# Kernel optimization log

Hardware: AMD Instinct MI355X
Metric: run time of the kernel (lower is better)

Reference implementation:

```python
import jax, jax.numpy as jnp
import numpy as np

B, CIN, COUT, K, SDIM, H, W = 16, 512, 512, 3, 512, 64, 64


def setup_inputs() -> dict:
    key = jax.random.key(0)
    k1, k2, k3, k4 = jax.random.split(key, 4)
    return {
        "x": jax.random.normal(k1, (B, CIN, H, W), dtype=jnp.float32),
        "style": jax.random.normal(k2, (B, SDIM), dtype=jnp.float32),
        "weight": jax.random.normal(k3, (COUT, CIN, K, K), dtype=jnp.float32),
        "style_w": jax.random.normal(k4, (CIN, SDIM), dtype=jnp.float32),
        "style_b": jnp.ones((CIN,), dtype=jnp.float32),  # bias.data.fill_(1.0)
    }


def reference(x, style, weight, style_w, style_b):
    batch, in_ch, h, w_size = x.shape
    out_ch, _, ks, _ = weight.shape
    pad = ks // 2
    # EqualizedLinear: runtime weight scaling by 1/sqrt(fan_in)
    lin_scale = 1.0 / np.sqrt(style_w.shape[1])
    s = style @ (style_w * lin_scale).T + style_b  # [B, Cin]
    # modulate
    conv_scale = 1.0 / np.sqrt(in_ch * ks * ks)
    wmod = (weight[None] * conv_scale) * s[:, None, :, None, None]  # [B,Cout,Cin,k,k]
    # demodulate
    dcoef = jax.lax.rsqrt(jnp.sum(jnp.square(wmod), axis=(2, 3, 4)) + 1e-8)  # [B,Cout]
    wmod = wmod * dcoef[:, :, None, None, None]
    # grouped conv with groups = batch
    x_r = x.reshape(1, batch * in_ch, h, w_size)
    w_r = wmod.reshape(batch * out_ch, in_ch, ks, ks)
    out = jax.lax.conv_general_dilated(
        x_r, w_r,
        window_strides=(1, 1),
        padding=[(pad, pad), (pad, pad)],
        dimension_numbers=("NCHW", "OIHW", "NCHW"),
        feature_group_count=batch,
    )
    return out.reshape(batch, out_ch, h, w_size)
```

## Files before the change

### kernel.cpp

```cpp
#include <hip/hip_runtime.h>
#include <math.h>

#define B 16
#define CIN 512
#define COUT 512
#define SDIM 512
#define H 64
#define W 64

typedef short s16x8 __attribute__((ext_vector_type(8)));
typedef float f32x4 __attribute__((ext_vector_type(4)));
typedef float f32x16 __attribute__((ext_vector_type(16)));

__device__ __constant__ float LIN_SCALE  = 0.04419417382415922f;
__device__ __constant__ float CONV_SCALE = 0.014731391274719742f;

__device__ __forceinline__ ushort f2bf(float f) {
  unsigned u = __float_as_uint(f);
  return (ushort)((u + 0x7FFFu + ((u >> 16) & 1u)) >> 16);
}

#define GLOAD16(g, l)                                           \
  __builtin_amdgcn_global_load_lds(                             \
      (const __attribute__((address_space(1))) unsigned*)(g),   \
      (__attribute__((address_space(3))) unsigned*)(l), 16, 0, 0)

__global__ __launch_bounds__(256) void prep1_kernel(
    const float* __restrict__ w, const float* __restrict__ style,
    const float* __restrict__ style_w, const float* __restrict__ style_b,
    ushort* __restrict__ wt, float* __restrict__ wsq, float* __restrict__ s,
    float* __restrict__ s2) {
  const int tid = threadIdx.x;
  if (blockIdx.x < 512) {
    const int u = blockIdx.x * 256 + tid;
    const int e = u & 7;
    const int chunk = (u >> 3) & 31;
    const int co = u >> 8;
    const float2* wp = (const float2*)(
        w + ((size_t)co * 512 + chunk * 16 + e * 2) * 9);
    float wv[18];
#pragma unroll
    for (int i = 0; i < 9; ++i) {
      float2 v = wp[i];
      wv[2 * i] = v.x;
      wv[2 * i + 1] = v.y;
    }
    {
      float q0 = 0.f, q1 = 0.f;
#pragma unroll
      for (int k = 0; k < 9; ++k) {
        q0 += wv[k] * wv[k];
        q1 += wv[9 + k] * wv[9 + k];
      }
      *(float2*)(wsq + (size_t)co * 512 + chunk * 16 + e * 2) =
          make_float2(q0, q1);
    }
    const int cb = co >> 6, co64 = co & 63;
    ushort* dst = wt + (size_t)chunk * 73728 + (size_t)cb * 9216 +
                  (size_t)(e >> 2) * 512 + (size_t)co64 * 8 + (e & 3) * 2;
#pragma unroll
    for (int j = 0; j < 9; ++j) {
      unsigned pk = (unsigned)f2bf(wv[j]) | ((unsigned)f2bf(wv[9 + j]) << 16);
      *(unsigned*)(dst + (size_t)j * 1024) = pk;
    }
  } else {
    const int bb = blockIdx.x - 512;
    __shared__ float st[SDIM];
    st[tid] = style[bb * SDIM + tid];
    st[tid + 256] = style[bb * SDIM + tid + 256];
    __syncthreads();
#pragma unroll
    for (int half = 0; half < 2; ++half) {
      const int ci = tid + half * 256;
      const float4* wr =
          reinterpret_cast<const float4*>(style_w + (size_t)ci * SDIM);
      float acc = 0.f;
#pragma unroll 4
      for (int k = 0; k < SDIM / 4; ++k) {
        float4 wv = wr[k];
        acc += st[4 * k + 0] * wv.x + st[4 * k + 1] * wv.y +
               st[4 * k + 2] * wv.z + st[4 * k + 3] * wv.w;
      }
      float v = acc * LIN_SCALE + style_b[ci];
      s[bb * CIN + ci] = v;
      s2[bb * CIN + ci] = v * v;
    }
  }
}

__global__ __launch_bounds__(256) void prep2_kernel(
    const float* __restrict__ x, const float* __restrict__ smod,
    const float* __restrict__ s2, const float* __restrict__ wsq,
    ushort* __restrict__ xp, float* __restrict__ outscale) {
  const int tid = threadIdx.x;
  if (blockIdx.x < 16384) {
    const int blk = blockIdx.x;
    const int gr = blk & 63, cp = (blk >> 6) & 15, b = blk >> 10;
    __shared__ float xt[32][65];
    __shared__ float sm[32];
    if (tid < 32) sm[tid] = smod[b * 512 + cp * 32 + tid];
    {
      const int ci = tid >> 3, cq = tid & 7;
      const float4* rp = (const float4*)(
          x + (((size_t)b * 512 + cp * 32 + ci) * 64 + gr) * 64 + cq * 8);
      float4 a = rp[0], c2 = rp[1];
      float* row = &xt[ci][cq * 8];
      row[0] = a.x; row[1] = a.y; row[2] = a.z; row[3] = a.w;
      row[4] = c2.x; row[5] = c2.y; row[6] = c2.z; row[7] = c2.w;
    }
    __syncthreads();
    const int c = tid & 63, o = tid >> 6;
    s16x8 p;
#pragma unroll
    for (int i = 0; i < 8; ++i)
      p[i] = (short)f2bf(xt[o * 8 + i][c] * sm[o * 8 + i]);
    const int chunk = cp * 2 + (o >> 1), oct = o & 1;
    *(s16x8*)(xp + (size_t)b * 2097152 + (size_t)chunk * 65536 +
              oct * 32768 + gr * 512 + c * 8) = p;
  } else {
    const int b = blockIdx.x - 16384;
    __shared__ float sh[CIN];
    sh[tid] = s2[b * CIN + tid];
    sh[tid + 256] = s2[b * CIN + tid + 256];
    __syncthreads();
#pragma unroll
    for (int half = 0; half < 2; ++half) {
      const int co = tid + half * 256;
      const float4* wr =
          reinterpret_cast<const float4*>(wsq + (size_t)co * CIN);
      float acc = 0.f;
#pragma unroll 4
      for (int k = 0; k < CIN / 4; ++k) {
        float4 wv = wr[k];
        acc += sh[4 * k + 0] * wv.x + sh[4 * k + 1] * wv.y +
               sh[4 * k + 2] * wv.z + sh[4 * k + 3] * wv.w;
      }
      float d = rsqrtf(acc * CONV_SCALE * CONV_SCALE + 1e-8f);
      outscale[b * COUT + co] = d * CONV_SCALE;
    }
  }
}

#define CBUF_WS 18432
#define CBUF_XS 21120
#define XS_BASE 36864
#define DLDS9 79104

__global__ __launch_bounds__(256, 2) void conv_mfma9_kernel(
    const ushort* __restrict__ wt, const ushort* __restrict__ xp,
    const float* __restrict__ outscale, float* __restrict__ out) {
  extern __shared__ char smem[];

  const int tid = threadIdx.x;
  const int hb = blockIdx.x;
  const int cb = blockIdx.y;
  const int b  = blockIdx.z;
  const int h0 = hb * 8, co0 = cb * 64;
  const int lane = tid & 63, wid = tid >> 6;
  const int l31 = lane & 31, hi = lane >> 5;

  {
    s16x8* p = (s16x8*)(smem + XS_BASE);
    for (int e = tid; e < 2640; e += 256) p[e] = (s16x8)0;
  }

  f32x16 acc[2][2][2];
#pragma unroll
  for (int rr = 0; rr < 2; ++rr)
#pragma unroll
    for (int mt = 0; mt < 2; ++mt)
#pragma unroll
      for (int nt = 0; nt < 2; ++nt) acc[rr][mt][nt] = (f32x16)0.f;

  int aoff[2];
#pragma unroll
  for (int mt = 0; mt < 2; ++mt)
    aoff[mt] = hi * 1024 + (mt * 32 + l31) * 16;
  int boff[3][2];
#pragma unroll
  for (int kw = 0; kw < 3; ++kw)
#pragma unroll
    for (int nt = 0; nt < 2; ++nt)
      boff[kw][nt] = hi * 10560 + (nt * 32 + l31 + kw) * 16;

  const char* wsrc0 = (const char*)wt + (size_t)cb * 18432;
  const char* xsrc0 = (const char*)xp + (size_t)b * 4194304;

  auto stage = [&](int chunk, int buf) {
    const char* wsrc = wsrc0 + (size_t)chunk * 147456;
    const char* xsrc = xsrc0 + (size_t)chunk * 131072;
    char* wd = smem + buf * CBUF_WS;
    char* xd = smem + XS_BASE + buf * CBUF_XS;
#pragma unroll
    for (int p = 0; p < 4; ++p)
      GLOAD16(wsrc + p * 4096 + tid * 16, wd + p * 4096 + tid * 16);
    if (tid < 128)
      GLOAD16(wsrc + 16384 + tid * 16, wd + 16384 + tid * 16);
#pragma unroll
    for (int p = 0; p < 5; ++p) {
      int e = p * 4 + wid;
      int oct = (e >= 10) ? 1 : 0;
      int r = e - oct * 10;
      int gr = h0 - 1 + r;
      if ((unsigned)gr < 64u)
        GLOAD16(xsrc + oct * 65536 + gr * 1024 + lane * 16,
                xd + oct * 10560 + r * 1056 + 16 + lane * 16);
    }
  };

  auto compute = [&](int buf) {
    const char* wb2 = smem + buf * CBUF_WS;
    const char* xb2 = smem + XS_BASE + buf * CBUF_XS + 2 * wid * 1056;
#pragma unroll
    for (int kw = 0; kw < 3; ++kw) {
      s16x8 bf[4][2];
#pragma unroll
      for (int q = 0; q < 4; ++q)
#pragma unroll
        for (int nt = 0; nt < 2; ++nt)
          bf[q][nt] = *(const s16x8*)(xb2 + q * 1056 + boff[kw][nt]);
#pragma unroll
      for (int kh = 0; kh < 3; ++kh) {
        const char* wj = wb2 + (kh * 3 + kw) * 2048;
        s16x8 af0 = *(const s16x8*)(wj + aoff[0]);
        s16x8 af1 = *(const s16x8*)(wj + aoff[1]);
#pragma unroll
        for (int rr = 0; rr < 2; ++rr)
#pragma unroll
          for (int nt = 0; nt < 2; ++nt) {
            acc[rr][0][nt] = __builtin_amdgcn_mfma_f32_32x32x16_bf16(
                af0, bf[rr + kh][nt], acc[rr][0][nt], 0, 0, 0);
            acc[rr][1][nt] = __builtin_amdgcn_mfma_f32_32x32x16_bf16(
                af1, bf[rr + kh][nt], acc[rr][1][nt], 0, 0, 0);
          }
      }
    }
  };

  __syncthreads();
  stage(0, 0);

  for (int c = 0; c < 32; ++c) {
    const int buf = c & 1;
    __syncthreads();
    if (c + 1 < 32) stage(c + 1, buf ^ 1);
    compute(buf);
  }

#pragma unroll
  for (int mt = 0; mt < 2; ++mt) {
#pragma unroll
    for (int reg = 0; reg < 16; ++reg) {
      const int row = (reg & 3) + 8 * (reg >> 2) + 4 * hi;
      const int co = co0 + mt * 32 + row;
      const float osc = outscale[b * COUT + co];
      float* obase = out + ((size_t)b * COUT + co) * H * W;
#pragma unroll
      for (int rr = 0; rr < 2; ++rr) {
        const int h = h0 + 2 * wid + rr;
#pragma unroll
        for (int nt = 0; nt < 2; ++nt)
          obase[h * W + nt * 32 + l31] = acc[rr][mt][nt][reg] * osc;
      }
    }
  }
}

__global__ __launch_bounds__(256, 2) void conv_mfma_kernel(
    const float* __restrict__ x, const float* __restrict__ weight,
    const float* __restrict__ s, const float* __restrict__ outscale,
    float* __restrict__ out) {
  __shared__ ushort xs[6][66][32];
  __shared__ ushort ws[9][64][32];

  const int tid = threadIdx.x;
  const int hb = blockIdx.x;
  const int cb = blockIdx.y;
  const int b  = blockIdx.z;
  const int h0 = hb * 4;
  const int co0 = cb * 64;
  const int lane = tid & 63;
  const int wid = tid >> 6;
  const int l15 = lane & 15;
  const int l4  = lane >> 4;

  f32x4 acc[4][4];
#pragma unroll
  for (int mt = 0; mt < 4; ++mt)
#pragma unroll
    for (int nt = 0; nt < 4; ++nt) acc[mt][nt] = (f32x4)0.f;

  const int wq = tid & 3;
  const int wco = tid >> 2;

  for (int c0 = 0; c0 < CIN; c0 += 32) {
    {
      const float4* wp = reinterpret_cast<const float4*>(
          weight + ((size_t)(co0 + wco) * CIN + c0 + wq * 8) * 9);
      float wv[72];
#pragma unroll
      for (int t = 0; t < 18; ++t) {
        float4 v = wp[t];
        wv[4 * t + 0] = v.x; wv[4 * t + 1] = v.y;
        wv[4 * t + 2] = v.z; wv[4 * t + 3] = v.w;
      }
      float sv[8];
#pragma unroll
      for (int i = 0; i < 8; ++i) sv[i] = s[b * CIN + c0 + wq * 8 + i];
#pragma unroll
      for (int j = 0; j < 9; ++j) {
        s16x8 p;
#pragma unroll
        for (int i = 0; i < 8; ++i)
          p[i] = (short)f2bf(wv[i * 9 + j] * sv[i]);
        *reinterpret_cast<s16x8*>(&ws[j][wco][wq * 8]) = p;
      }
    }
#pragma unroll
    for (int it = 0; it < 7; ++it) {
      int e = tid + it * 256;
      if (e < 6 * 66 * 4) {
        int q = e & 3;
        int t2 = e >> 2;
        int cc = t2 % 66;
        int r = t2 / 66;
        int gr = h0 - 1 + r;
        int gc = cc - 1;
        s16x8 p;
        if ((unsigned)gr < H && (unsigned)gc < W) {
          const float* xp2 =
              x + (((size_t)b * CIN + c0 + q * 8) * H + gr) * W + gc;
#pragma unroll
          for (int i = 0; i < 8; ++i) p[i] = (short)f2bf(xp2[(size_t)i * H * W]);
        } else {
#pragma unroll
          for (int i = 0; i < 8; ++i) p[i] = 0;
        }
        *reinterpret_cast<s16x8*>(&xs[r][cc][q * 8]) = p;
      }
    }
    __syncthreads();

#pragma unroll
    for (int kh = 0; kh < 3; ++kh) {
#pragma unroll
      for (int kw = 0; kw < 3; ++kw) {
        const int j = kh * 3 + kw;
        s16x8 af[4], bf[4];
#pragma unroll
        for (int mt = 0; mt < 4; ++mt)
          af[mt] = *reinterpret_cast<const s16x8*>(
              &ws[j][mt * 16 + l15][l4 * 8]);
#pragma unroll
        for (int nt = 0; nt < 4; ++nt)
          bf[nt] = *reinterpret_cast<const s16x8*>(
              &xs[wid + kh][nt * 16 + l15 + kw][l4 * 8]);
#pragma unroll
        for (int mt = 0; mt < 4; ++mt)
#pragma unroll
          for (int nt = 0; nt < 4; ++nt)
            acc[mt][nt] = __builtin_amdgcn_mfma_f32_16x16x32_bf16(
                af[mt], bf[nt], acc[mt][nt], 0, 0, 0);
      }
    }
    __syncthreads();
  }

  const int h = h0 + wid;
#pragma unroll
  for (int mt = 0; mt < 4; ++mt) {
#pragma unroll
    for (int r = 0; r < 4; ++r) {
      const int co = co0 + mt * 16 + l4 * 4 + r;
      const float osc = outscale[b * COUT + co];
      float* orow = out + (((size_t)b * COUT + co) * H + h) * W;
#pragma unroll
      for (int nt = 0; nt < 4; ++nt)
        orow[nt * 16 + l15] = acc[mt][nt][r] * osc;
    }
  }
}

extern "C" void kernel_launch(void* const* d_in, const int* in_sizes, int n_in,
                              void* d_out, int out_size, void* d_ws,
                              size_t ws_size, hipStream_t stream) {
  const float* x = (const float*)d_in[0];
  const float* style = (const float*)d_in[1];
  const float* weight = (const float*)d_in[2];
  const float* style_w = (const float*)d_in[3];
  const float* style_b = (const float*)d_in[4];
  float* out = (float*)d_out;

  char* wsb = (char*)d_ws;
  float* s = (float*)(wsb + 0);
  float* s2 = (float*)(wsb + 32768);
  float* wsq = (float*)(wsb + 65536);
  float* outscale = (float*)(wsb + 1114112);
  ushort* wt = (ushort*)(wsb + 1146880);
  ushort* xp = (ushort*)(wsb + 5865472);
  const size_t NEED = 72974336;

  hipError_t attr_ok = hipFuncSetAttribute(
      reinterpret_cast<const void*>(conv_mfma9_kernel),
      hipFuncAttributeMaxDynamicSharedMemorySize, DLDS9);

  prep1_kernel<<<528, 256, 0, stream>>>(weight, style, style_w, style_b, wt,
                                        wsq, s, s2);
  if (attr_ok == hipSuccess && ws_size >= NEED) {
    prep2_kernel<<<16400, 256, 0, stream>>>(x, s, s2, wsq, xp, outscale);
    conv_mfma9_kernel<<<dim3(8, 8, 16), 256, DLDS9, stream>>>(wt, xp, outscale,
                                                              out);
  } else {
    prep2_kernel<<<16400, 256, 0, stream>>>(x, s, s2, wsq, xp, outscale);
    conv_mfma_kernel<<<dim3(16, 8, 16), 256, 0, stream>>>(x, weight, s,
                                                          outscale, out);
  }
}
```

Baseline: 339.7 us.

## Split style projection, merge weight/x packing, fold demod coefficient into conv epilogue

Style modulation now runs in its own small kernel, and weight packing and x packing are merged into one launch. The per-output demodulation coefficient is no longer a separate pass. Each conv block computes it in its epilogue from wsq and s2 held in shared memory. This cuts the launch chain from two prep kernels to two lighter ones and removes the outscale round trip, at the cost of recomputing dcoef in every one of the 8 h-blocks per (co-block, batch) tile.

New measurement: 320.9 us. -5.5%, faster.

```diff
diff --git a/kernel.cpp b/kernel.cpp
--- a/kernel.cpp
+++ b/kernel.cpp
@@ -25,11 +25,33 @@
       (const __attribute__((address_space(1))) unsigned*)(g),   \
       (__attribute__((address_space(3))) unsigned*)(l), 16, 0, 0)
 
-__global__ __launch_bounds__(256) void prep1_kernel(
-    const float* __restrict__ w, const float* __restrict__ style,
-    const float* __restrict__ style_w, const float* __restrict__ style_b,
-    ushort* __restrict__ wt, float* __restrict__ wsq, float* __restrict__ s,
+__global__ __launch_bounds__(512) void style_mod_kernel(
+    const float* __restrict__ style, const float* __restrict__ style_w,
+    const float* __restrict__ style_b, float* __restrict__ s,
     float* __restrict__ s2) {
+  const int b = blockIdx.x;
+  const int ci = threadIdx.x;
+  __shared__ float st[SDIM];
+  st[ci] = style[b * SDIM + ci];
+  __syncthreads();
+
+  const float4* wr = reinterpret_cast<const float4*>(style_w + (size_t)ci * SDIM);
+  float acc = 0.f;
+#pragma unroll 4
+  for (int k = 0; k < SDIM / 4; ++k) {
+    float4 wv = wr[k];
+    acc += st[4 * k + 0] * wv.x + st[4 * k + 1] * wv.y +
+           st[4 * k + 2] * wv.z + st[4 * k + 3] * wv.w;
+  }
+  float v = acc * LIN_SCALE + style_b[ci];
+  s[b * CIN + ci] = v;
+  s2[b * CIN + ci] = v * v;
+}
+
+__global__ __launch_bounds__(256) void pack_kernel(
+    const float* __restrict__ w, const float* __restrict__ x,
+    const float* __restrict__ smod, ushort* __restrict__ wt,
+    float* __restrict__ wsq, ushort* __restrict__ xp) {
   const int tid = threadIdx.x;
   if (blockIdx.x < 512) {
     const int u = blockIdx.x * 256 + tid;
@@ -64,37 +86,7 @@
       *(unsigned*)(dst + (size_t)j * 1024) = pk;
     }
   } else {
-    const int bb = blockIdx.x - 512;
-    __shared__ float st[SDIM];
-    st[tid] = style[bb * SDIM + tid];
-    st[tid + 256] = style[bb * SDIM + tid + 256];
-    __syncthreads();
-#pragma unroll
-    for (int half = 0; half < 2; ++half) {
-      const int ci = tid + half * 256;
-      const float4* wr =
-          reinterpret_cast<const float4*>(style_w + (size_t)ci * SDIM);
-      float acc = 0.f;
-#pragma unroll 4
-      for (int k = 0; k < SDIM / 4; ++k) {
-        float4 wv = wr[k];
-        acc += st[4 * k + 0] * wv.x + st[4 * k + 1] * wv.y +
-               st[4 * k + 2] * wv.z + st[4 * k + 3] * wv.w;
-      }
-      float v = acc * LIN_SCALE + style_b[ci];
-      s[bb * CIN + ci] = v;
-      s2[bb * CIN + ci] = v * v;
-    }
-  }
-}
-
-__global__ __launch_bounds__(256) void prep2_kernel(
-    const float* __restrict__ x, const float* __restrict__ smod,
-    const float* __restrict__ s2, const float* __restrict__ wsq,
-    ushort* __restrict__ xp, float* __restrict__ outscale) {
-  const int tid = threadIdx.x;
-  if (blockIdx.x < 16384) {
-    const int blk = blockIdx.x;
+    const int blk = blockIdx.x - 512;
     const int gr = blk & 63, cp = (blk >> 6) & 15, b = blk >> 10;
     __shared__ float xt[32][65];
     __shared__ float sm[32];
@@ -117,27 +109,6 @@
     const int chunk = cp * 2 + (o >> 1), oct = o & 1;
     *(s16x8*)(xp + (size_t)b * 2097152 + (size_t)chunk * 65536 +
               oct * 32768 + gr * 512 + c * 8) = p;
-  } else {
-    const int b = blockIdx.x - 16384;
-    __shared__ float sh[CIN];
-    sh[tid] = s2[b * CIN + tid];
-    sh[tid + 256] = s2[b * CIN + tid + 256];
-    __syncthreads();
-#pragma unroll
-    for (int half = 0; half < 2; ++half) {
-      const int co = tid + half * 256;
-      const float4* wr =
-          reinterpret_cast<const float4*>(wsq + (size_t)co * CIN);
-      float acc = 0.f;
-#pragma unroll 4
-      for (int k = 0; k < CIN / 4; ++k) {
-        float4 wv = wr[k];
-        acc += sh[4 * k + 0] * wv.x + sh[4 * k + 1] * wv.y +
-               sh[4 * k + 2] * wv.z + sh[4 * k + 3] * wv.w;
-      }
-      float d = rsqrtf(acc * CONV_SCALE * CONV_SCALE + 1e-8f);
-      outscale[b * COUT + co] = d * CONV_SCALE;
-    }
   }
 }
 
@@ -148,7 +119,8 @@
 
 __global__ __launch_bounds__(256, 2) void conv_mfma9_kernel(
     const ushort* __restrict__ wt, const ushort* __restrict__ xp,
-    const float* __restrict__ outscale, float* __restrict__ out) {
+    const float* __restrict__ wsq, const float* __restrict__ s2,
+    float* __restrict__ out) {
   extern __shared__ char smem[];
 
   const int tid = threadIdx.x;
@@ -247,13 +219,36 @@
     compute(buf);
   }
 
+  __syncthreads();
+  float* s2sh = (float*)smem;
+  float* oscsh = (float*)(smem + 2048);
+  s2sh[tid] = s2[b * CIN + tid];
+  s2sh[tid + 256] = s2[b * CIN + tid + 256];
+  __syncthreads();
+  {
+    const int co = tid >> 2, q = tid & 3;
+    const float4* wr = (const float4*)(wsq + (size_t)(co0 + co) * CIN);
+    float a = 0.f;
+#pragma unroll
+    for (int k = 0; k < 32; ++k) {
+      float4 v = wr[q + k * 4];
+      const float* sp = s2sh + (q + k * 4) * 4;
+      a += v.x * sp[0] + v.y * sp[1] + v.z * sp[2] + v.w * sp[3];
+    }
+    a += __shfl_xor(a, 1);
+    a += __shfl_xor(a, 2);
+    if (q == 0)
+      oscsh[co] = CONV_SCALE * rsqrtf(a * CONV_SCALE * CONV_SCALE + 1e-8f);
+  }
+  __syncthreads();
+
 #pragma unroll
   for (int mt = 0; mt < 2; ++mt) {
 #pragma unroll
     for (int reg = 0; reg < 16; ++reg) {
       const int row = (reg & 3) + 8 * (reg >> 2) + 4 * hi;
       const int co = co0 + mt * 32 + row;
-      const float osc = outscale[b * COUT + co];
+      const float osc = oscsh[mt * 32 + row];
       float* obase = out + ((size_t)b * COUT + co) * H * W;
 #pragma unroll
       for (int rr = 0; rr < 2; ++rr) {
@@ -264,6 +259,27 @@
       }
     }
   }
+}
+
+__global__ __launch_bounds__(512) void dcoef_kernel(
+    const float* __restrict__ s2, const float* __restrict__ wsq,
+    float* __restrict__ outscale) {
+  const int b = blockIdx.x;
+  const int co = threadIdx.x;
+  __shared__ float sh[CIN];
+  sh[co] = s2[b * CIN + co];
+  __syncthreads();
+
+  const float4* wr = reinterpret_cast<const float4*>(wsq + (size_t)co * CIN);
+  float acc = 0.f;
+#pragma unroll 4
+  for (int k = 0; k < CIN / 4; ++k) {
+    float4 wv = wr[k];
+    acc += sh[4 * k + 0] * wv.x + sh[4 * k + 1] * wv.y +
+           sh[4 * k + 2] * wv.z + sh[4 * k + 3] * wv.w;
+  }
+  float d = rsqrtf(acc * CONV_SCALE * CONV_SCALE + 1e-8f);
+  outscale[b * COUT + co] = d * CONV_SCALE;
 }
 
 __global__ __launch_bounds__(256, 2) void conv_mfma_kernel(
@@ -404,14 +420,14 @@
       reinterpret_cast<const void*>(conv_mfma9_kernel),
       hipFuncAttributeMaxDynamicSharedMemorySize, DLDS9);
 
-  prep1_kernel<<<528, 256, 0, stream>>>(weight, style, style_w, style_b, wt,
-                                        wsq, s, s2);
+  style_mod_kernel<<<B, 512, 0, stream>>>(style, style_w, style_b, s, s2);
+  pack_kernel<<<16896, 256, 0, stream>>>(weight, x, s, wt, wsq, xp);
+
   if (attr_ok == hipSuccess && ws_size >= NEED) {
-    prep2_kernel<<<16400, 256, 0, stream>>>(x, s, s2, wsq, xp, outscale);
-    conv_mfma9_kernel<<<dim3(8, 8, 16), 256, DLDS9, stream>>>(wt, xp, outscale,
+    conv_mfma9_kernel<<<dim3(8, 8, 16), 256, DLDS9, stream>>>(wt, xp, wsq, s2,
                                                               out);
   } else {
-    prep2_kernel<<<16400, 256, 0, stream>>>(x, s, s2, wsq, xp, outscale);
+    dcoef_kernel<<<B, 512, 0, stream>>>(s2, wsq, outscale);
     conv_mfma_kernel<<<dim3(16, 8, 16), 256, 0, stream>>>(x, weight, s,
                                                           outscale, out);
   }
```
